# Performance work log

Hardware: AMD Instinct MI355X
Metric: run time of the kernel (lower is better)

Reference implementation:

```python
import jax, jax.numpy as jnp
import numpy as np

B, CI, CO = 4, 64, 128
N_IN, N_OUT, K, P, H = 65536, 16384, 9, 4, 32
EPS = 1e-5


def setup_inputs() -> dict:
    key = jax.random.key(0)
    ks = jax.random.split(key, 16)
    inp = {
        "x": jax.random.normal(ks[0], (B, CI, N_IN), jnp.float32),
        "off1": jax.random.normal(ks[1], (N_OUT, K, 2), jnp.float32),
        "off2": jax.random.normal(ks[2], (N_OUT, K, 2), jnp.float32),
        "nbr1": jax.random.randint(ks[3], (N_OUT, K), 0, N_IN),
        "nbr2": jax.random.randint(ks[4], (N_OUT, K), 0, N_OUT),
        "pool_idx": jax.random.randint(ks[5], (N_OUT, P), 0, N_IN),
        # shared weight_net: 2 -> H -> 1 MLP producing per-neighbor interp weight
        "wn_w1": jax.random.normal(ks[6], (2, H), jnp.float32) * 0.5,
        "wn_b1": jnp.zeros((H,), jnp.float32),
        "wn_w2": jax.random.normal(ks[7], (H, 1), jnp.float32) * 0.5,
        "wn_b2": jnp.zeros((1,), jnp.float32),
        # conv weights [C_out, C_in, K]
        "W1": jax.random.normal(ks[8], (CO, CI, K), jnp.float32) * (1.0 / np.sqrt(CI * K)),
        "W2": jax.random.normal(ks[9], (CO, CO, K), jnp.float32) * (1.0 / np.sqrt(CO * K)),
        # batchnorm affine params
        "bn1_g": jnp.ones((CO,), jnp.float32),
        "bn1_b": jnp.zeros((CO,), jnp.float32),
        "bn2_g": jnp.ones((CO,), jnp.float32),
        "bn2_b": jnp.zeros((CO,), jnp.float32),
        # 1x1 expand conv
        "exp_w": jax.random.normal(ks[10], (CO, CI), jnp.float32) * (1.0 / np.sqrt(CI)),
        "exp_b": jnp.zeros((CO,), jnp.float32),
    }
    return inp


def _weight_net(off, w1, b1, w2, b2):
    # off: [M, K, 2] -> interp weights [M, K]
    h = jax.nn.relu(off @ w1 + b1)
    return (h @ w2 + b2)[..., 0]


def _interp_conv(x, W, idx, a):
    # x: [B, Ci, N_in], idx: [M, K], a: [M, K], W: [Co, Ci, K]
    g = x[:, :, idx]  # gather -> [B, Ci, M, K]
    return jnp.einsum("bimk,mk,oik->bom", g, a, W)


def _bn(x, g, b):
    # training-mode BatchNorm1d over (batch, points) per channel
    m = x.mean(axis=(0, 2), keepdims=True)
    v = x.var(axis=(0, 2), keepdims=True)
    return (x - m) * jax.lax.rsqrt(v + EPS) * g[None, :, None] + b[None, :, None]


def reference(x, off1, off2, wn_w1, wn_b1, wn_w2, wn_b2, W1, W2,
              bn1_g, bn1_b, bn2_g, bn2_b, exp_w, exp_b,
              nbr1, nbr2, pool_idx):
    a1 = _weight_net(off1, wn_w1, wn_b1, wn_w2, wn_b2)  # [M, K]
    out = _interp_conv(x, W1, nbr1, a1)                  # [B, Co, M]
    out = jax.nn.relu(_bn(out, bn1_g, bn1_b))
    a2 = _weight_net(off2, wn_w1, wn_b1, wn_w2, wn_b2)
    out = _interp_conv(out, W2, nbr2, a2)
    out = _bn(out, bn2_g, bn2_b)
    # downsample identity: AvgPoolNG over 4 nearest in_locs per out_loc
    identity = x[:, :, pool_idx].mean(axis=-1)           # [B, Ci, M]
    # expand channels: 1x1 conv
    identity = jnp.einsum("oi,bim->bom", exp_w, identity) + exp_b[None, :, None]
    return jax.nn.relu(out + identity)
```

## Files before the change

kernel.cpp:

```cpp
#include <hip/hip_runtime.h>
#include <hip/hip_bf16.h>

#define B_    4
#define CI_   64
#define CO_   128
#define NIN_  65536
#define NOUT_ 16384
#define KK_   9
#define PP_   4
#define HH_   32

typedef _Float16 f16x8 __attribute__((ext_vector_type(8)));
typedef _Float16 f16x4 __attribute__((ext_vector_type(4)));
typedef float    f32x4 __attribute__((ext_vector_type(4)));


__global__ void zero_kernel(float* p, int n) {
    int i = blockIdx.x * 256 + threadIdx.x;
    if (i < n) p[i] = 0.f;
}

__global__ void wnet_kernel(const float* __restrict__ off1, const float* __restrict__ off2,
                            const float* __restrict__ w1, const float* __restrict__ b1,
                            const float* __restrict__ w2, const float* __restrict__ b2,
                            float* __restrict__ a1, float* __restrict__ a2) {
    int idx = blockIdx.x * 256 + threadIdx.x;
    if (idx >= NOUT_ * KK_) return;
    float x0 = off1[idx*2+0], x1 = off1[idx*2+1];
    float y0 = off2[idx*2+0], y1 = off2[idx*2+1];
    float bias2 = b2[0];
    float s1 = bias2, s2 = bias2;
    #pragma unroll
    for (int h = 0; h < HH_; ++h) {
        float wh0 = w1[h], wh1 = w1[HH_+h], bh = b1[h], vh = w2[h];
        s1 += fmaxf(x0*wh0 + x1*wh1 + bh, 0.f) * vh;
        s2 += fmaxf(y0*wh0 + y1*wh1 + bh, 0.f) * vh;
    }
    a1[idx] = s1;
    a2[idx] = s2;
}

template<int CIN>
__global__ void wpack_kernel(const float* __restrict__ W, _Float16* __restrict__ Wf) {
    constexpr int NSLAB = (CIN/64) * KK_;
    int f = blockIdx.x * 256 + threadIdx.x;
    if (f >= NSLAB * 8192) return;
    int j   = f & 7;
    int l   = (f >> 3) & 63;
    int ot  = (f >> 9) & 7;
    int kap = (f >> 12) & 1;
    int s   = f >> 13;
    int o   = ot*16 + (l & 15);
    int kel = kap*32 + ((l >> 4) & 3)*8 + j;
    int k, i;
    if (CIN == 64) { k = s; i = kel; }
    else           { k = s >> 1; i = ((s & 1) << 6) + kel; }
    Wf[f] = (_Float16)W[((size_t)o*CIN + i)*KK_ + k];
}

__global__ void epack_kernel(const float* __restrict__ E, _Float16* __restrict__ Ef) {
    int f = blockIdx.x * 256 + threadIdx.x;
    if (f >= 8192) return;
    int j   = f & 7;
    int l   = (f >> 3) & 63;
    int ot  = (f >> 9) & 7;
    int kap = (f >> 12) & 1;
    int o   = ot*16 + (l & 15);
    int i   = kap*32 + ((l >> 4) & 3)*8 + j;
    Ef[f] = (_Float16)E[o*64 + i];
}

__global__ void xtrans_kernel(const float* __restrict__ x, _Float16* __restrict__ xT) {
    __shared__ float tile[64][65];
    int p0 = blockIdx.x * 64;
    int b  = blockIdx.y;
    int t  = threadIdx.x;
    #pragma unroll
    for (int r = 0; r < 16; ++r) {
        int f = r*256 + t;
        int i = f >> 6, pp = f & 63;
        tile[i][pp] = x[((size_t)(b*CI_ + i))*NIN_ + p0 + pp];
    }
    __syncthreads();
    #pragma unroll
    for (int r = 0; r < 16; ++r) {
        int f = r*256 + t;
        int pp = f >> 6, i = f & 63;
        xT[((size_t)(p0+pp)*B_ + b)*CI_ + i] = (_Float16)tile[i][pp];
    }
}

__global__ __launch_bounds__(256) void bnreduce_kernel(const float* __restrict__ pbuf,
                                                       float* __restrict__ stats) {
    int t = threadIdx.x;
    float s = 0.f;
    int base = blockIdx.x * 16;
    #pragma unroll
    for (int b = 0; b < 16; ++b)
        s += pbuf[(size_t)(base + b)*256 + t];
    atomicAdd(&stats[t], s);
}

__global__ void bnparams_kernel(const float* __restrict__ gsum, const float* __restrict__ gsq,
                                const float* __restrict__ g, const float* __restrict__ bb,
                                const float* __restrict__ eb,
                                float* __restrict__ scbi) {
    int o = threadIdx.x;
    const float inv_n = 1.f / (B_ * NOUT_);
    float mean = gsum[o] * inv_n;
    float var  = gsq[o] * inv_n - mean*mean;
    float sc   = g[o] * rsqrtf(var + 1e-5f);
    scbi[o]       = sc;
    scbi[128 + o] = bb[o] - mean*sc + eb[o];
}

__global__ __launch_bounds__(256) void bnrelu_kernel(_Float16* __restrict__ t,
                                                     const float* __restrict__ scbi) {
    __shared__ float ssc[128], sbi[128];
    if (threadIdx.x < 128) {
        ssc[threadIdx.x] = scbi[threadIdx.x];
        sbi[threadIdx.x] = scbi[128 + threadIdx.x];
    }
    __syncthreads();
    size_t idx = ((size_t)blockIdx.x*256 + threadIdx.x) * 8;
    int o0 = (int)(idx & 127);
    f16x8 v = *(f16x8*)(t + idx);
    #pragma unroll
    for (int e = 0; e < 8; ++e) {
        float f = (float)v[e] * ssc[o0+e] + sbi[o0+e];
        v[e] = (_Float16)fmaxf(f, 0.f);
    }
    *(f16x8*)(t + idx) = v;
}

template<int CIN, int NSLAB>
__global__ __launch_bounds__(256, 2) void conv_mfma_kernel(
    const _Float16* __restrict__ in,
    const _Float16* __restrict__ Wf,
    const int*      __restrict__ nbr,
    const float*    __restrict__ amk,
    _Float16*       __restrict__ outh,
    float*          __restrict__ pbuf)
{
    __shared__ _Float16 Gs[128*64];
    const int t    = threadIdx.x;
    const int lane = t & 63;
    const int wid  = t >> 6;
    const int wr   = wid >> 1, wc = wid & 1;
    const int m0   = blockIdx.x * 32;
    const int l15 = lane & 15, l4 = lane >> 4, l7 = lane & 7;
    const int srow = t >> 1;
    const int sh   = t & 1;
    const int sm   = m0 + (srow >> 2);
    const int sb   = srow & 3;

    f32x4 acc[4][4];
    #pragma unroll
    for (int c = 0; c < 4; ++c)
        #pragma unroll
        for (int j = 0; j < 4; ++j)
            acc[c][j] = (f32x4){0.f, 0.f, 0.f, 0.f};

    for (int s = 0; s < NSLAB; ++s) {
        const int k    = (CIN == 64) ? s : (s >> 1);
        const int ioff = (CIN == 64) ? 0 : ((s & 1) << 6);
        f16x8 aF[2][4];
        #pragma unroll
        for (int kap = 0; kap < 2; ++kap)
            #pragma unroll
            for (int c = 0; c < 4; ++c)
                aF[kap][c] = *(const f16x8*)(Wf +
                    ((size_t)((s*2 + kap)*8 + (wr*4 + c))*64 + lane)*8);
        const int   p  = nbr[sm*KK_ + k];
        const float av = amk[sm*KK_ + k];
        const _Float16 hs = (_Float16)av;
        const _Float16* src = in + ((size_t)p*B_ + sb)*CIN + ioff + sh*32;
        f16x8 g[4];
        #pragma unroll
        for (int q = 0; q < 4; ++q) g[q] = *(const f16x8*)(src + q*8);
        __syncthreads();
        #pragma unroll
        for (int q = 0; q < 4; ++q) {
            f16x8 v = g[q];
            #pragma unroll
            for (int e = 0; e < 8; ++e) v[e] = v[e] * hs;
            const int c4 = sh*4 + q;
            *(f16x8*)(Gs + srow*64 + ((c4 ^ (srow & 7)) << 3)) = v;
        }
        __syncthreads();
        #pragma unroll
        for (int kap = 0; kap < 2; ++kap) {
            f16x8 bF[4];
            #pragma unroll
            for (int jt = 0; jt < 4; ++jt) {
                const int row = wc*64 + jt*16 + l15;
                const int ch  = (kap*4 + l4) ^ l7;
                bF[jt] = *(const f16x8*)(Gs + row*64 + (ch << 3));
            }
            #pragma unroll
            for (int c = 0; c < 4; ++c)
                #pragma unroll
                for (int jt = 0; jt < 4; ++jt)
                    acc[c][jt] = __builtin_amdgcn_mfma_f32_16x16x32_f16(
                        aF[kap][c], bF[jt], acc[c][jt], 0, 0, 0);
        }
    }
    __syncthreads();
    float* red = (float*)Gs;
    #pragma unroll
    for (int c = 0; c < 4; ++c) {
        #pragma unroll
        for (int r = 0; r < 4; ++r) {
            float s = acc[c][0][r] + acc[c][1][r] + acc[c][2][r] + acc[c][3][r];
            float q = acc[c][0][r]*acc[c][0][r] + acc[c][1][r]*acc[c][1][r]
                    + acc[c][2][r]*acc[c][2][r] + acc[c][3][r]*acc[c][3][r];
            #pragma unroll
            for (int msk = 1; msk <= 8; msk <<= 1) {
                s += __shfl_xor(s, msk);
                q += __shfl_xor(q, msk);
            }
            if (l15 == 0) {
                const int o = wr*64 + c*16 + l4*4 + r;
                red[wc*256 + o]       = s;
                red[wc*256 + 128 + o] = q;
            }
        }
    }
    __syncthreads();
    pbuf[(size_t)blockIdx.x*256 + t] = red[t] + red[256 + t];
    #pragma unroll
    for (int c = 0; c < 4; ++c) {
        const int o = wr*64 + c*16 + l4*4;
        #pragma unroll
        for (int jt = 0; jt < 4; ++jt) {
            const int n = wc*64 + jt*16 + l15;
            f16x4 h;
            #pragma unroll
            for (int r = 0; r < 4; ++r) h[r] = (_Float16)acc[c][jt][r];
            *(f16x4*)(outh + ((size_t)(m0*B_) + n)*CO_ + o) = h;
        }
    }
}

__global__ __launch_bounds__(256, 4) void final_mfma_kernel(
    const _Float16* __restrict__ xh,
    const _Float16* __restrict__ out2T,
    const int*      __restrict__ pool_idx,
    const _Float16* __restrict__ Ef,
    const float*    __restrict__ scbi2,
    float*          __restrict__ out)
{
    __shared__ _Float16 Gs[64*64];
    const int t    = threadIdx.x;
    const int lane = t & 63;
    const int wid  = t >> 6;
    const int wr   = wid >> 1, wc = wid & 1;
    const int m0   = blockIdx.x * 16;
    const int l15 = lane & 15, l4 = lane >> 4, l7 = lane & 7;

    {
        const int srow = t >> 2;
        const int sq   = t & 3;
        const int m    = m0 + (srow & 15);
        const int b    = srow >> 4;
        const int4 pidx = *(const int4*)(pool_idx + m*4);
        const _Float16* r0 = xh + ((size_t)pidx.x*B_ + b)*CI_ + sq*16;
        const _Float16* r1 = xh + ((size_t)pidx.y*B_ + b)*CI_ + sq*16;
        const _Float16* r2 = xh + ((size_t)pidx.z*B_ + b)*CI_ + sq*16;
        const _Float16* r3 = xh + ((size_t)pidx.w*B_ + b)*CI_ + sq*16;
        #pragma unroll
        for (int q = 0; q < 2; ++q) {
            f16x8 v  = *(const f16x8*)(r0 + q*8);
            f16x8 v1 = *(const f16x8*)(r1 + q*8);
            f16x8 v2 = *(const f16x8*)(r2 + q*8);
            f16x8 v3 = *(const f16x8*)(r3 + q*8);
            v = v + v1 + v2 + v3;
            #pragma unroll
            for (int e = 0; e < 8; ++e) v[e] = v[e] * (_Float16)0.25f;
            const int c4 = sq*2 + q;
            *(f16x8*)(Gs + srow*64 + ((c4 ^ (srow & 7)) << 3)) = v;
        }
    }
    __syncthreads();

    f32x4 acc[4][2];
    #pragma unroll
    for (int c = 0; c < 4; ++c)
        #pragma unroll
        for (int j = 0; j < 2; ++j)
            acc[c][j] = (f32x4){0.f, 0.f, 0.f, 0.f};
    #pragma unroll
    for (int kap = 0; kap < 2; ++kap) {
        f16x8 aF[4], bF[2];
        #pragma unroll
        for (int c = 0; c < 4; ++c)
            aF[c] = *(const f16x8*)(Ef + ((size_t)((kap*8 + wr*4 + c)*64 + lane))*8);
        #pragma unroll
        for (int jt = 0; jt < 2; ++jt) {
            const int row = wc*32 + jt*16 + l15;
            const int ch  = (kap*4 + l4) ^ l7;
            bF[jt] = *(const f16x8*)(Gs + row*64 + (ch << 3));
        }
        #pragma unroll
        for (int c = 0; c < 4; ++c)
            #pragma unroll
            for (int jt = 0; jt < 2; ++jt)
                acc[c][jt] = __builtin_amdgcn_mfma_f32_16x16x32_f16(
                    aF[c], bF[jt], acc[c][jt], 0, 0, 0);
    }

    const int m = m0 + l15;
    #pragma unroll
    for (int c = 0; c < 4; ++c) {
        const int o = wr*64 + c*16 + l4*4;
        const float4 sc4 = *(const float4*)(scbi2 + o);
        const float4 bi4 = *(const float4*)(scbi2 + 128 + o);
        #pragma unroll
        for (int jt = 0; jt < 2; ++jt) {
            const int b = wc*2 + jt;
            const f16x4 v2 = *(const f16x4*)(out2T + ((size_t)(m*B_ + b))*CO_ + o);
            float res0 = fmaxf(acc[c][jt][0] + (float)v2[0]*sc4.x + bi4.x, 0.f);
            float res1 = fmaxf(acc[c][jt][1] + (float)v2[1]*sc4.y + bi4.y, 0.f);
            float res2 = fmaxf(acc[c][jt][2] + (float)v2[2]*sc4.z + bi4.z, 0.f);
            float res3 = fmaxf(acc[c][jt][3] + (float)v2[3]*sc4.w + bi4.w, 0.f);
            out[((size_t)(b*CO_ + o + 0))*NOUT_ + m] = res0;
            out[((size_t)(b*CO_ + o + 1))*NOUT_ + m] = res1;
            out[((size_t)(b*CO_ + o + 2))*NOUT_ + m] = res2;
            out[((size_t)(b*CO_ + o + 3))*NOUT_ + m] = res3;
        }
    }
}

extern "C" void kernel_launch(void* const* d_in, const int* in_sizes, int n_in,
                              void* d_out, int out_size, void* d_ws, size_t ws_size,
                              hipStream_t stream) {
    const float* x        = (const float*)d_in[0];
    const float* off1     = (const float*)d_in[1];
    const float* off2     = (const float*)d_in[2];
    const int*   nbr1     = (const int*)  d_in[3];
    const int*   nbr2     = (const int*)  d_in[4];
    const int*   pool_idx = (const int*)  d_in[5];
    const float* wn_w1    = (const float*)d_in[6];
    const float* wn_b1    = (const float*)d_in[7];
    const float* wn_w2    = (const float*)d_in[8];
    const float* wn_b2    = (const float*)d_in[9];
    const float* W1       = (const float*)d_in[10];
    const float* W2       = (const float*)d_in[11];
    const float* bn1_g    = (const float*)d_in[12];
    const float* bn1_b    = (const float*)d_in[13];
    const float* bn2_g    = (const float*)d_in[14];
    const float* bn2_b    = (const float*)d_in[15];
    const float* exp_w    = (const float*)d_in[16];
    const float* exp_b    = (const float*)d_in[17];
    float* out = (float*)d_out;

    char* ws = (char*)d_ws;
    float* a1      = (float*)ws;  ws += (size_t)NOUT_*KK_*4;
    float* a2      = (float*)ws;  ws += (size_t)NOUT_*KK_*4;
    float* scbi1   = (float*)ws;  ws += 256*4;
    float* scbi2   = (float*)ws;  ws += 256*4;
    float* stats   = (float*)ws;  ws += 640*4;
    float* pbuf    = (float*)ws;  ws += (size_t)512*256*4;
    _Float16* Wf1  = (_Float16*)ws; ws += (size_t)9*8192*2;
    _Float16* Wf2  = (_Float16*)ws; ws += (size_t)18*8192*2;
    _Float16* Ef   = (_Float16*)ws; ws += (size_t)8192*2;
    _Float16* xh   = (_Float16*)ws; ws += (size_t)NIN_*B_*CI_*2;
    _Float16* o1h  = (_Float16*)ws; ws += (size_t)NOUT_*B_*CO_*2;
    _Float16* o2h  = (_Float16*)ws; ws += (size_t)NOUT_*B_*CO_*2;

    float* sum1  = stats;       float* sq1 = stats + 128;
    float* sum2  = stats + 256; float* sq2 = stats + 384;
    float* fzero = stats + 512;

    zero_kernel<<<3, 256, 0, stream>>>(stats, 640);
    wnet_kernel<<<(NOUT_*KK_ + 255)/256, 256, 0, stream>>>(off1, off2, wn_w1, wn_b1, wn_w2, wn_b2, a1, a2);
    wpack_kernel<CI_><<<(9*8192 + 255)/256, 256, 0, stream>>>(W1, Wf1);
    wpack_kernel<CO_><<<(18*8192 + 255)/256, 256, 0, stream>>>(W2, Wf2);
    epack_kernel<<<32, 256, 0, stream>>>(exp_w, Ef);
    xtrans_kernel<<<dim3(NIN_/64, B_), 256, 0, stream>>>(x, xh);

    conv_mfma_kernel<CI_, 9><<<NOUT_/32, 256, 0, stream>>>(xh, Wf1, nbr1, a1, o1h, pbuf);
    bnreduce_kernel<<<32, 256, 0, stream>>>(pbuf, sum1);
    bnparams_kernel<<<1, 128, 0, stream>>>(sum1, sq1, bn1_g, bn1_b, fzero, scbi1);
    bnrelu_kernel<<<4096, 256, 0, stream>>>(o1h, scbi1);

    conv_mfma_kernel<CO_, 18><<<NOUT_/32, 256, 0, stream>>>(o1h, Wf2, nbr2, a2, o2h, pbuf);
    bnreduce_kernel<<<32, 256, 0, stream>>>(pbuf, sum2);
    bnparams_kernel<<<1, 128, 0, stream>>>(sum2, sq2, bn2_g, bn2_b, exp_b, scbi2);

    final_mfma_kernel<<<NOUT_/16, 256, 0, stream>>>(xh, o2h, pool_idx, Ef, scbi2, out);
}
```

Before: 128.4 us.

## Restructure conv kernel with double-buffered LDS, register prefetch, and smaller tiles

```diff
diff --git a/kernel.cpp b/kernel.cpp
--- a/kernel.cpp
+++ b/kernel.cpp
@@ -83,10 +83,14 @@
     }
     __syncthreads();
     #pragma unroll
-    for (int r = 0; r < 16; ++r) {
-        int f = r*256 + t;
-        int pp = f >> 6, i = f & 63;
-        xT[((size_t)(p0+pp)*B_ + b)*CI_ + i] = (_Float16)tile[i][pp];
+    for (int r = 0; r < 2; ++r) {
+        int f  = r*256 + t;
+        int pp = f >> 3;
+        int i0 = (f & 7) * 8;
+        f16x8 v;
+        #pragma unroll
+        for (int e = 0; e < 8; ++e) v[e] = (_Float16)tile[i0+e][pp];
+        *(f16x8*)(xT + ((size_t)(p0+pp)*B_ + b)*CI_ + i0) = v;
     }
 }
 
@@ -94,9 +98,9 @@
                                                        float* __restrict__ stats) {
     int t = threadIdx.x;
     float s = 0.f;
-    int base = blockIdx.x * 16;
-    #pragma unroll
-    for (int b = 0; b < 16; ++b)
+    int base = blockIdx.x * 32;
+    #pragma unroll
+    for (int b = 0; b < 32; ++b)
         s += pbuf[(size_t)(base + b)*256 + t];
     atomicAdd(&stats[t], s);
 }
@@ -133,8 +137,8 @@
     *(f16x8*)(t + idx) = v;
 }
 
-template<int CIN, int NSLAB>
-__global__ __launch_bounds__(256, 2) void conv_mfma_kernel(
+template<int CIN>
+__global__ __launch_bounds__(256, CIN == 64 ? 4 : 3) void conv_mfma_kernel(
     const _Float16* __restrict__ in,
     const _Float16* __restrict__ Wf,
     const int*      __restrict__ nbr,
@@ -142,78 +146,90 @@
     _Float16*       __restrict__ outh,
     float*          __restrict__ pbuf)
 {
-    __shared__ _Float16 Gs[128*64];
+    constexpr int NKAP = CIN/32;
+    __shared__ _Float16 Gs[2][64*CIN];
     const int t    = threadIdx.x;
     const int lane = t & 63;
     const int wid  = t >> 6;
     const int wr   = wid >> 1, wc = wid & 1;
-    const int m0   = blockIdx.x * 32;
+    const int m0   = blockIdx.x * 16;
     const int l15 = lane & 15, l4 = lane >> 4, l7 = lane & 7;
-    const int srow = t >> 1;
-    const int sh   = t & 1;
+    const int srow = t >> 2;
+    const int sq   = t & 3;
+    const int sb   = srow & 3;
     const int sm   = m0 + (srow >> 2);
-    const int sb   = srow & 3;
-
-    f32x4 acc[4][4];
+
+    int   pn[KK_];
+    float pa[KK_];
+    #pragma unroll
+    for (int k = 0; k < KK_; ++k) { pn[k] = nbr[sm*KK_ + k]; pa[k] = amk[sm*KK_ + k]; }
+
+    f32x4 acc[4][2];
     #pragma unroll
     for (int c = 0; c < 4; ++c)
         #pragma unroll
-        for (int j = 0; j < 4; ++j)
+        for (int j = 0; j < 2; ++j)
             acc[c][j] = (f32x4){0.f, 0.f, 0.f, 0.f};
 
-    for (int s = 0; s < NSLAB; ++s) {
-        const int k    = (CIN == 64) ? s : (s >> 1);
-        const int ioff = (CIN == 64) ? 0 : ((s & 1) << 6);
-        f16x8 aF[2][4];
-        #pragma unroll
-        for (int kap = 0; kap < 2; ++kap)
+    f16x8 greg[NKAP];
+    {
+        const _Float16* src = in + ((size_t)pn[0]*B_ + sb)*CIN + sq*(CIN/4);
+        #pragma unroll
+        for (int q = 0; q < NKAP; ++q) greg[q] = *(const f16x8*)(src + q*8);
+    }
+
+    #pragma unroll
+    for (int s = 0; s < KK_; ++s) {
+        const _Float16 hs = (_Float16)pa[s];
+        #pragma unroll
+        for (int q = 0; q < NKAP; ++q) {
+            f16x8 v = greg[q];
+            #pragma unroll
+            for (int e = 0; e < 8; ++e) v[e] = v[e] * hs;
+            const int c4 = sq*NKAP + q;
+            *(f16x8*)(&Gs[s&1][srow*CIN + ((c4 ^ (srow & 7)) << 3)]) = v;
+        }
+        __syncthreads();
+        f16x8 gn[NKAP];
+        if (s + 1 < KK_) {
+            const _Float16* src = in + ((size_t)pn[s+1]*B_ + sb)*CIN + sq*(CIN/4);
+            #pragma unroll
+            for (int q = 0; q < NKAP; ++q) gn[q] = *(const f16x8*)(src + q*8);
+        }
+        #pragma unroll
+        for (int kap = 0; kap < NKAP; ++kap) {
+            f16x8 aF[4], bF[2];
+            const _Float16* wbase = Wf + ((size_t)(s*NKAP + kap)*8*64)*8;
             #pragma unroll
             for (int c = 0; c < 4; ++c)
-                aF[kap][c] = *(const f16x8*)(Wf +
-                    ((size_t)((s*2 + kap)*8 + (wr*4 + c))*64 + lane)*8);
-        const int   p  = nbr[sm*KK_ + k];
-        const float av = amk[sm*KK_ + k];
-        const _Float16 hs = (_Float16)av;
-        const _Float16* src = in + ((size_t)p*B_ + sb)*CIN + ioff + sh*32;
-        f16x8 g[4];
-        #pragma unroll
-        for (int q = 0; q < 4; ++q) g[q] = *(const f16x8*)(src + q*8);
-        __syncthreads();
-        #pragma unroll
-        for (int q = 0; q < 4; ++q) {
-            f16x8 v = g[q];
-            #pragma unroll
-            for (int e = 0; e < 8; ++e) v[e] = v[e] * hs;
-            const int c4 = sh*4 + q;
-            *(f16x8*)(Gs + srow*64 + ((c4 ^ (srow & 7)) << 3)) = v;
-        }
-        __syncthreads();
-        #pragma unroll
-        for (int kap = 0; kap < 2; ++kap) {
-            f16x8 bF[4];
-            #pragma unroll
-            for (int jt = 0; jt < 4; ++jt) {
-                const int row = wc*64 + jt*16 + l15;
+                aF[c] = *(const f16x8*)(wbase + (((wr*4 + c)*64 + lane) << 3));
+            #pragma unroll
+            for (int jt = 0; jt < 2; ++jt) {
+                const int row = wc*32 + jt*16 + l15;
                 const int ch  = (kap*4 + l4) ^ l7;
-                bF[jt] = *(const f16x8*)(Gs + row*64 + (ch << 3));
+                bF[jt] = *(const f16x8*)(&Gs[s&1][row*CIN + (ch << 3)]);
             }
             #pragma unroll
             for (int c = 0; c < 4; ++c)
                 #pragma unroll
-                for (int jt = 0; jt < 4; ++jt)
+                for (int jt = 0; jt < 2; ++jt)
                     acc[c][jt] = __builtin_amdgcn_mfma_f32_16x16x32_f16(
-                        aF[kap][c], bF[jt], acc[c][jt], 0, 0, 0);
-        }
-    }
+                        aF[c], bF[jt], acc[c][jt], 0, 0, 0);
+        }
+        if (s + 1 < KK_) {
+            #pragma unroll
+            for (int q = 0; q < NKAP; ++q) greg[q] = gn[q];
+        }
+    }
+
     __syncthreads();
     float* red = (float*)Gs;
     #pragma unroll
     for (int c = 0; c < 4; ++c) {
         #pragma unroll
         for (int r = 0; r < 4; ++r) {
-            float s = acc[c][0][r] + acc[c][1][r] + acc[c][2][r] + acc[c][3][r];
-            float q = acc[c][0][r]*acc[c][0][r] + acc[c][1][r]*acc[c][1][r]
-                    + acc[c][2][r]*acc[c][2][r] + acc[c][3][r]*acc[c][3][r];
+            float s = acc[c][0][r] + acc[c][1][r];
+            float q = acc[c][0][r]*acc[c][0][r] + acc[c][1][r]*acc[c][1][r];
             #pragma unroll
             for (int msk = 1; msk <= 8; msk <<= 1) {
                 s += __shfl_xor(s, msk);
@@ -232,8 +248,8 @@
     for (int c = 0; c < 4; ++c) {
         const int o = wr*64 + c*16 + l4*4;
         #pragma unroll
-        for (int jt = 0; jt < 4; ++jt) {
-            const int n = wc*64 + jt*16 + l15;
+        for (int jt = 0; jt < 2; ++jt) {
+            const int n = wc*32 + jt*16 + l15;
             f16x4 h;
             #pragma unroll
             for (int r = 0; r < 4; ++r) h[r] = (_Float16)acc[c][jt][r];
@@ -360,7 +376,7 @@
     float* scbi1   = (float*)ws;  ws += 256*4;
     float* scbi2   = (float*)ws;  ws += 256*4;
     float* stats   = (float*)ws;  ws += 640*4;
-    float* pbuf    = (float*)ws;  ws += (size_t)512*256*4;
+    float* pbuf    = (float*)ws;  ws += (size_t)1024*256*4;
     _Float16* Wf1  = (_Float16*)ws; ws += (size_t)9*8192*2;
     _Float16* Wf2  = (_Float16*)ws; ws += (size_t)18*8192*2;
     _Float16* Ef   = (_Float16*)ws; ws += (size_t)8192*2;
@@ -379,12 +395,12 @@
     epack_kernel<<<32, 256, 0, stream>>>(exp_w, Ef);
     xtrans_kernel<<<dim3(NIN_/64, B_), 256, 0, stream>>>(x, xh);
 
-    conv_mfma_kernel<CI_, 9><<<NOUT_/32, 256, 0, stream>>>(xh, Wf1, nbr1, a1, o1h, pbuf);
+    conv_mfma_kernel<CI_><<<NOUT_/16, 256, 0, stream>>>(xh, Wf1, nbr1, a1, o1h, pbuf);
     bnreduce_kernel<<<32, 256, 0, stream>>>(pbuf, sum1);
     bnparams_kernel<<<1, 128, 0, stream>>>(sum1, sq1, bn1_g, bn1_b, fzero, scbi1);
     bnrelu_kernel<<<4096, 256, 0, stream>>>(o1h, scbi1);
 
-    conv_mfma_kernel<CO_, 18><<<NOUT_/32, 256, 0, stream>>>(o1h, Wf2, nbr2, a2, o2h, pbuf);
+    conv_mfma_kernel<CO_><<<NOUT_/16, 256, 0, stream>>>(o1h, Wf2, nbr2, a2, o2h, pbuf);
     bnreduce_kernel<<<32, 256, 0, stream>>>(pbuf, sum2);
     bnparams_kernel<<<1, 128, 0, stream>>>(sum2, sq2, bn2_g, bn2_b, exp_b, scbi2);
 
```

Result: slower. 132.6 us (+3.3%).

## Merge prep kernels, fuse BN reduce+params, vectorize xtrans stores

Applied to the files above, without the earlier changes.

```diff
diff --git a/kernel.cpp b/kernel.cpp
--- a/kernel.cpp
+++ b/kernel.cpp
@@ -15,17 +15,11 @@
 typedef float    f32x4 __attribute__((ext_vector_type(4)));
 
 
-__global__ void zero_kernel(float* p, int n) {
-    int i = blockIdx.x * 256 + threadIdx.x;
-    if (i < n) p[i] = 0.f;
-}
-
-__global__ void wnet_kernel(const float* __restrict__ off1, const float* __restrict__ off2,
-                            const float* __restrict__ w1, const float* __restrict__ b1,
-                            const float* __restrict__ w2, const float* __restrict__ b2,
-                            float* __restrict__ a1, float* __restrict__ a2) {
-    int idx = blockIdx.x * 256 + threadIdx.x;
-    if (idx >= NOUT_ * KK_) return;
+__device__ __forceinline__ void wnet_body(int idx,
+        const float* __restrict__ off1, const float* __restrict__ off2,
+        const float* __restrict__ w1, const float* __restrict__ b1,
+        const float* __restrict__ w2, const float* __restrict__ b2,
+        float* __restrict__ a1, float* __restrict__ a2) {
     float x0 = off1[idx*2+0], x1 = off1[idx*2+1];
     float y0 = off2[idx*2+0], y1 = off2[idx*2+1];
     float bias2 = b2[0];
@@ -41,10 +35,8 @@
 }
 
 template<int CIN>
-__global__ void wpack_kernel(const float* __restrict__ W, _Float16* __restrict__ Wf) {
-    constexpr int NSLAB = (CIN/64) * KK_;
-    int f = blockIdx.x * 256 + threadIdx.x;
-    if (f >= NSLAB * 8192) return;
+__device__ __forceinline__ void wpack_body(int f, const float* __restrict__ W,
+                                           _Float16* __restrict__ Wf) {
     int j   = f & 7;
     int l   = (f >> 3) & 63;
     int ot  = (f >> 9) & 7;
@@ -58,16 +50,33 @@
     Wf[f] = (_Float16)W[((size_t)o*CIN + i)*KK_ + k];
 }
 
-__global__ void epack_kernel(const float* __restrict__ E, _Float16* __restrict__ Ef) {
-    int f = blockIdx.x * 256 + threadIdx.x;
-    if (f >= 8192) return;
-    int j   = f & 7;
-    int l   = (f >> 3) & 63;
-    int ot  = (f >> 9) & 7;
-    int kap = (f >> 12) & 1;
-    int o   = ot*16 + (l & 15);
-    int i   = kap*32 + ((l >> 4) & 3)*8 + j;
-    Ef[f] = (_Float16)E[o*64 + i];
+__global__ __launch_bounds__(256) void prep_kernel(
+        const float* __restrict__ off1, const float* __restrict__ off2,
+        const float* __restrict__ wn_w1, const float* __restrict__ wn_b1,
+        const float* __restrict__ wn_w2, const float* __restrict__ wn_b2,
+        const float* __restrict__ W1, const float* __restrict__ W2,
+        const float* __restrict__ exp_w,
+        float* __restrict__ a1, float* __restrict__ a2,
+        _Float16* __restrict__ Wf1, _Float16* __restrict__ Wf2,
+        _Float16* __restrict__ Ef) {
+    const int blk = blockIdx.x;
+    const int t   = threadIdx.x;
+    if (blk < 576) {
+        wnet_body(blk*256 + t, off1, off2, wn_w1, wn_b1, wn_w2, wn_b2, a1, a2);
+    } else if (blk < 576 + 288) {
+        wpack_body<CI_>((blk - 576)*256 + t, W1, Wf1);
+    } else if (blk < 576 + 288 + 576) {
+        wpack_body<CO_>((blk - 864)*256 + t, W2, Wf2);
+    } else {
+        int f = (blk - 1440)*256 + t;
+        int j   = f & 7;
+        int l   = (f >> 3) & 63;
+        int ot  = (f >> 9) & 7;
+        int kap = (f >> 12) & 1;
+        int o   = ot*16 + (l & 15);
+        int i   = kap*32 + ((l >> 4) & 3)*8 + j;
+        Ef[f] = (_Float16)exp_w[o*64 + i];
+    }
 }
 
 __global__ void xtrans_kernel(const float* __restrict__ x, _Float16* __restrict__ xT) {
@@ -83,35 +92,38 @@
     }
     __syncthreads();
     #pragma unroll
-    for (int r = 0; r < 16; ++r) {
-        int f = r*256 + t;
-        int pp = f >> 6, i = f & 63;
-        xT[((size_t)(p0+pp)*B_ + b)*CI_ + i] = (_Float16)tile[i][pp];
-    }
-}
-
-__global__ __launch_bounds__(256) void bnreduce_kernel(const float* __restrict__ pbuf,
-                                                       float* __restrict__ stats) {
-    int t = threadIdx.x;
+    for (int r = 0; r < 2; ++r) {
+        int f  = r*256 + t;
+        int pp = f >> 3;
+        int i0 = (f & 7) * 8;
+        f16x8 v;
+        #pragma unroll
+        for (int e = 0; e < 8; ++e) v[e] = (_Float16)tile[i0+e][pp];
+        *(f16x8*)(xT + ((size_t)(p0+pp)*B_ + b)*CI_ + i0) = v;
+    }
+}
+
+__global__ __launch_bounds__(256) void bnstats_kernel(const float* __restrict__ pbuf,
+                                                      const float* __restrict__ g,
+                                                      const float* __restrict__ bb,
+                                                      const float* __restrict__ eb,
+                                                      float* __restrict__ scbi) {
+    const int t = threadIdx.x;
     float s = 0.f;
-    int base = blockIdx.x * 16;
-    #pragma unroll
-    for (int b = 0; b < 16; ++b)
-        s += pbuf[(size_t)(base + b)*256 + t];
-    atomicAdd(&stats[t], s);
-}
-
-__global__ void bnparams_kernel(const float* __restrict__ gsum, const float* __restrict__ gsq,
-                                const float* __restrict__ g, const float* __restrict__ bb,
-                                const float* __restrict__ eb,
-                                float* __restrict__ scbi) {
-    int o = threadIdx.x;
-    const float inv_n = 1.f / (B_ * NOUT_);
-    float mean = gsum[o] * inv_n;
-    float var  = gsq[o] * inv_n - mean*mean;
-    float sc   = g[o] * rsqrtf(var + 1e-5f);
-    scbi[o]       = sc;
-    scbi[128 + o] = bb[o] - mean*sc + eb[o];
+    #pragma unroll 8
+    for (int b = 0; b < 512; ++b)
+        s += pbuf[(size_t)b*256 + t];
+    __shared__ float sm[256];
+    sm[t] = s;
+    __syncthreads();
+    if (t < 128) {
+        const float inv_n = 1.f / (B_ * NOUT_);
+        float mean = sm[t] * inv_n;
+        float var  = sm[128 + t] * inv_n - mean*mean;
+        float sc   = g[t] * rsqrtf(var + 1e-5f);
+        scbi[t]       = sc;
+        scbi[128 + t] = bb[t] - mean*sc + (eb ? eb[t] : 0.f);
+    }
 }
 
 __global__ __launch_bounds__(256) void bnrelu_kernel(_Float16* __restrict__ t,
@@ -359,7 +371,6 @@
     float* a2      = (float*)ws;  ws += (size_t)NOUT_*KK_*4;
     float* scbi1   = (float*)ws;  ws += 256*4;
     float* scbi2   = (float*)ws;  ws += 256*4;
-    float* stats   = (float*)ws;  ws += 640*4;
     float* pbuf    = (float*)ws;  ws += (size_t)512*256*4;
     _Float16* Wf1  = (_Float16*)ws; ws += (size_t)9*8192*2;
     _Float16* Wf2  = (_Float16*)ws; ws += (size_t)18*8192*2;
@@ -368,25 +379,16 @@
     _Float16* o1h  = (_Float16*)ws; ws += (size_t)NOUT_*B_*CO_*2;
     _Float16* o2h  = (_Float16*)ws; ws += (size_t)NOUT_*B_*CO_*2;
 
-    float* sum1  = stats;       float* sq1 = stats + 128;
-    float* sum2  = stats + 256; float* sq2 = stats + 384;
-    float* fzero = stats + 512;
-
-    zero_kernel<<<3, 256, 0, stream>>>(stats, 640);
-    wnet_kernel<<<(NOUT_*KK_ + 255)/256, 256, 0, stream>>>(off1, off2, wn_w1, wn_b1, wn_w2, wn_b2, a1, a2);
-    wpack_kernel<CI_><<<(9*8192 + 255)/256, 256, 0, stream>>>(W1, Wf1);
-    wpack_kernel<CO_><<<(18*8192 + 255)/256, 256, 0, stream>>>(W2, Wf2);
-    epack_kernel<<<32, 256, 0, stream>>>(exp_w, Ef);
+    prep_kernel<<<1472, 256, 0, stream>>>(off1, off2, wn_w1, wn_b1, wn_w2, wn_b2,
+                                          W1, W2, exp_w, a1, a2, Wf1, Wf2, Ef);
     xtrans_kernel<<<dim3(NIN_/64, B_), 256, 0, stream>>>(x, xh);
 
     conv_mfma_kernel<CI_, 9><<<NOUT_/32, 256, 0, stream>>>(xh, Wf1, nbr1, a1, o1h, pbuf);
-    bnreduce_kernel<<<32, 256, 0, stream>>>(pbuf, sum1);
-    bnparams_kernel<<<1, 128, 0, stream>>>(sum1, sq1, bn1_g, bn1_b, fzero, scbi1);
+    bnstats_kernel<<<1, 256, 0, stream>>>(pbuf, bn1_g, bn1_b, nullptr, scbi1);
     bnrelu_kernel<<<4096, 256, 0, stream>>>(o1h, scbi1);
 
     conv_mfma_kernel<CO_, 18><<<NOUT_/32, 256, 0, stream>>>(o1h, Wf2, nbr2, a2, o2h, pbuf);
-    bnreduce_kernel<<<32, 256, 0, stream>>>(pbuf, sum2);
-    bnparams_kernel<<<1, 128, 0, stream>>>(sum2, sq2, bn2_g, bn2_b, exp_b, scbi2);
+    bnstats_kernel<<<1, 256, 0, stream>>>(pbuf, bn2_g, bn2_b, exp_b, scbi2);
 
     final_mfma_kernel<<<NOUT_/16, 256, 0, stream>>>(xh, o2h, pool_idx, Ef, scbi2, out);
 }
```

Result: slower. 156.7 us (+22.0%).
